# Optimization experiments

Measured on AMD Instinct MI355X. Metric: run time of the kernel, lower is better.

The kernel has to match this reference:

```python
import jax, jax.numpy as jnp
import numpy as np

N_NODES = 100000
N_EDGES = 1600000
D_FEAT = 32


def setup_inputs() -> dict:
    key = jax.random.key(0)
    kx, ke = jax.random.split(key)
    x = jax.random.normal(kx, (N_NODES, D_FEAT), dtype=jnp.float32)
    edge_index = jax.random.randint(ke, (2, N_EDGES), 0, N_NODES, dtype=jnp.int64)
    return {"x": x, "edge_index": edge_index}


def reference(x, edge_index):
    # flow='source_to_target': messages flow from edge_index[0] (j, source)
    # to edge_index[1] (i, target).
    src = edge_index[0]  # [E] source node per edge (j)
    dst = edge_index[1]  # [E] target node per edge (i)
    # __lift__: gather source-node features per edge -> message(x_j) = x_j
    msgs = jnp.take(x, src, axis=0)  # [E, D]
    # aggregate with aggr='add': scatter-sum messages onto target nodes
    out = jax.ops.segment_sum(msgs, dst, num_segments=x.shape[0])  # [N, D]
    # update: identity
    return out
```

## Files before the change

kernel.cpp:

```cpp
#include <hip/hip_runtime.h>


#define D_FEAT 32
#define BKT_SHIFT 7
#define BKT_NODES 128
#define CAPSH 4
#define CAP (1 << CAPSH)
#define ECAP 4096
#define OVFCAP 65536
typedef unsigned int u32;

__global__ void __launch_bounds__(512)
k_scatter4(const int* __restrict__ src, const int* __restrict__ dst,
           u32* __restrict__ cnt, u32* __restrict__ bin,
           u32* __restrict__ ovf, u32* __restrict__ ovf_cnt,
           int n_edges, int nb, int nsub, int chunk) {
    extern __shared__ u32 smem[];
    u32* s_stage = smem;
    u32* s_cur   = smem + ((size_t)nb << CAPSH);
    int blk = blockIdx.x, t = threadIdx.x;
    for (int i = t; i < nb; i += 512) s_cur[i] = 0u;
    __syncthreads();
    int beg = blk * chunk, end = min(beg + chunk, n_edges);
    for (int e = beg + t; e < end; e += 512) {
        u32 d = (u32)dst[e];
        u32 b = d >> BKT_SHIFT;
        u32 pos = atomicAdd(&s_cur[b], 1u);
        u32 packed = (u32)src[e] | ((d & (BKT_NODES - 1)) << 17);
        if (pos < (u32)CAP) {
            s_stage[(b << CAPSH) + pos] = packed;
        } else {
            u32 g = atomicAdd(ovf_cnt, 1u);
            if (g < OVFCAP) { ovf[2 * g] = packed; ovf[2 * g + 1] = b; }
        }
    }
    __syncthreads();
    {
        int nquads = (nb << CAPSH) >> 2;
        uint4* gq = (uint4*)(bin + (((size_t)blk * nb) << CAPSH));
        const uint4* sq = (const uint4*)s_stage;
        for (int i = t; i < nquads; i += 512) gq[i] = sq[i];
    }
    u32* row = cnt + (size_t)blk * nb;
    for (int i = t; i < nb; i += 512) row[i] = min(s_cur[i], (u32)CAP);
}

__global__ void __launch_bounds__(512)
k_gather4(const float* __restrict__ x, const u32* __restrict__ cnt,
          const u32* __restrict__ bin, const u32* __restrict__ ovf,
          const u32* __restrict__ ovf_cnt, float* __restrict__ out,
          int n_nodes, int nb, int nsub) {
    __shared__ u32 s_cnt[512];
    __shared__ u32 s_sb[512];
    __shared__ u32 s_base[513];
    __shared__ u32 s_ent[ECAP];
    __shared__ u32 s_srt[ECAP];
    __shared__ u32 s_off[BKT_NODES + 1];
    __shared__ u32 s_cur[BKT_NODES];
    __shared__ u32 s_scan[BKT_NODES];
    int b = blockIdx.x, t = threadIdx.x;
    int node0 = b * BKT_NODES;
    const float4* x4 = (const float4*)x;
    const uint4* bin4 = (const uint4*)bin;
    int q = t & 7;
    int n0 = t >> 3;
    float4 a0 = make_float4(0.f, 0.f, 0.f, 0.f);
    float4 a1 = make_float4(0.f, 0.f, 0.f, 0.f);

    u32 c = 0u;
    if (t < nsub) c = min(cnt[(size_t)t * nb + b], (u32)CAP);
    s_cnt[t] = c;
    s_sb[t] = c;
    __syncthreads();
    for (int off = 1; off < 512; off <<= 1) {
        u32 y = (t >= off) ? s_sb[t - off] : 0u;
        __syncthreads();
        if (t >= off) s_sb[t] += y;
        __syncthreads();
    }
    s_base[t] = s_sb[t] - c;
    if (t == 511) s_base[512] = s_sb[511];
    __syncthreads();

    int subA = 0;
    u32 baseA = 0u;
    while (subA < nsub) {
        int lo = subA + 1, hi = nsub;
        while (lo < hi) {
            int mid = (lo + hi + 1) >> 1;
            if (s_base[mid] - baseA <= (u32)ECAP) lo = mid; else hi = mid - 1;
        }
        int subB = lo;
        int m = (int)(s_base[subB] - baseA);

        {
            int quads = (subB - subA) << (CAPSH - 2);
            for (int i = t; i < quads; i += 512) {
                int sub = subA + (i >> (CAPSH - 2));
                int k4 = i & ((1 << (CAPSH - 2)) - 1);
                int slot0 = k4 << 2;
                u32 cn = s_cnt[sub];
                if ((u32)slot0 < cn) {
                    uint4 v = bin4[(((size_t)sub * nb + b) << (CAPSH - 2)) + k4];
                    u32 base = (s_base[sub] - baseA) + slot0;
                    s_ent[base] = v.x;
                    if ((u32)(slot0 + 1) < cn) s_ent[base + 1] = v.y;
                    if ((u32)(slot0 + 2) < cn) s_ent[base + 2] = v.z;
                    if ((u32)(slot0 + 3) < cn) s_ent[base + 3] = v.w;
                }
            }
        }
        if (t < BKT_NODES) s_cur[t] = 0u;
        __syncthreads();

        for (int i = t; i < m; i += 512) atomicAdd(&s_cur[s_ent[i] >> 17], 1u);
        __syncthreads();
        u32 v = 0u;
        if (t < BKT_NODES) { v = s_cur[t]; s_scan[t] = v; }
        __syncthreads();
        for (int off = 1; off < BKT_NODES; off <<= 1) {
            u32 y = 0u;
            if (t < BKT_NODES && t >= off) y = s_scan[t - off];
            __syncthreads();
            if (t < BKT_NODES && t >= off) s_scan[t] += y;
            __syncthreads();
        }
        if (t < BKT_NODES) { u32 ex = s_scan[t] - v; s_off[t] = ex; s_cur[t] = ex; }
        if (t == BKT_NODES - 1) s_off[BKT_NODES] = s_scan[BKT_NODES - 1];
        __syncthreads();
        for (int i = t; i < m; i += 512) {
            u32 p = s_ent[i];
            u32 pos = atomicAdd(&s_cur[p >> 17], 1u);
            s_srt[pos] = p & 0x1FFFFu;
        }
        __syncthreads();

        {
            u32 j = s_off[n0], j1 = s_off[n0 + 1];
            for (; j + 3 < j1; j += 4) {
                float4 xa = x4[(size_t)s_srt[j] * 8 + q];
                float4 xb = x4[(size_t)s_srt[j + 1] * 8 + q];
                float4 xc = x4[(size_t)s_srt[j + 2] * 8 + q];
                float4 xd = x4[(size_t)s_srt[j + 3] * 8 + q];
                a0.x += xa.x + xb.x + xc.x + xd.x;
                a0.y += xa.y + xb.y + xc.y + xd.y;
                a0.z += xa.z + xb.z + xc.z + xd.z;
                a0.w += xa.w + xb.w + xc.w + xd.w;
            }
            for (; j < j1; ++j) {
                float4 xa = x4[(size_t)s_srt[j] * 8 + q];
                a0.x += xa.x; a0.y += xa.y; a0.z += xa.z; a0.w += xa.w;
            }
            j = s_off[n0 + 64]; j1 = s_off[n0 + 65];
            for (; j + 3 < j1; j += 4) {
                float4 xa = x4[(size_t)s_srt[j] * 8 + q];
                float4 xb = x4[(size_t)s_srt[j + 1] * 8 + q];
                float4 xc = x4[(size_t)s_srt[j + 2] * 8 + q];
                float4 xd = x4[(size_t)s_srt[j + 3] * 8 + q];
                a1.x += xa.x + xb.x + xc.x + xd.x;
                a1.y += xa.y + xb.y + xc.y + xd.y;
                a1.z += xa.z + xb.z + xc.z + xd.z;
                a1.w += xa.w + xb.w + xc.w + xd.w;
            }
            for (; j < j1; ++j) {
                float4 xa = x4[(size_t)s_srt[j] * 8 + q];
                a1.x += xa.x; a1.y += xa.y; a1.z += xa.z; a1.w += xa.w;
            }
        }
        __syncthreads();
        subA = subB;
        baseA = s_base[subB];
    }

    u32 novf = min(*ovf_cnt, (u32)OVFCAP);
    for (u32 i = 0; i < novf; ++i) {
        if (ovf[2 * i + 1] == (u32)b) {
            u32 p = ovf[2 * i];
            u32 dl = p >> 17;
            if (dl == (u32)n0 || dl == (u32)(n0 + 64)) {
                float4 xv = x4[(size_t)(p & 0x1FFFFu) * 8 + q];
                if (dl == (u32)n0) { a0.x += xv.x; a0.y += xv.y; a0.z += xv.z; a0.w += xv.w; }
                else               { a1.x += xv.x; a1.y += xv.y; a1.z += xv.z; a1.w += xv.w; }
            }
        }
    }

    float4* o4 = (float4*)out;
    if (node0 + n0 < n_nodes)      o4[(size_t)node0 * 8 + t] = a0;
    if (node0 + n0 + 64 < n_nodes) o4[(size_t)node0 * 8 + 512 + t] = a1;
}


__global__ void __launch_bounds__(256)
mp_zero_kernel(float* __restrict__ out, int n) {
    int i = blockIdx.x * blockDim.x + threadIdx.x;
    if (i < n) out[i] = 0.0f;
}

__global__ void __launch_bounds__(256)
mp_scatter_kernel(const float* __restrict__ x, const int* __restrict__ src,
                  const int* __restrict__ dst, float* __restrict__ out,
                  int n_edges) {
    int idx = blockIdx.x * blockDim.x + threadIdx.x;
    if (idx >= n_edges * 8) return;
    int e = idx >> 3;
    int c = idx & 7;
    const float4 v = *reinterpret_cast<const float4*>(x + (size_t)src[e] * D_FEAT + c * 4);
    float* o = out + (size_t)dst[e] * D_FEAT + c * 4;
    unsafeAtomicAdd(o + 0, v.x);
    unsafeAtomicAdd(o + 1, v.y);
    unsafeAtomicAdd(o + 2, v.z);
    unsafeAtomicAdd(o + 3, v.w);
}


extern "C" void kernel_launch(void* const* d_in, const int* in_sizes, int n_in,
                              void* d_out, int out_size, void* d_ws, size_t ws_size,
                              hipStream_t stream) {
    const float* x = (const float*)d_in[0];
    const int* edge_index = (const int*)d_in[1];
    int n_edges = in_sizes[1] / 2;
    const int* src = edge_index;
    const int* dst = edge_index + n_edges;
    float* out = (float*)d_out;
    int n_nodes = out_size / D_FEAT;

    int nb = (n_nodes + BKT_NODES - 1) >> BKT_SHIFT;

    size_t sc_lds = ((size_t)nb * CAP + nb) * sizeof(u32);

    if (n_nodes <= (1 << 17) && sc_lds <= 64 * 1024) {
        const int ncand[3] = {512, 384, 256};
        for (int ci = 0; ci < 3; ++ci) {
            int nsub = ncand[ci];
            int chunk = (n_edges + nsub - 1) / nsub;
            size_t need = ((size_t)nsub * nb
                           + 16
                           + 2 * (size_t)OVFCAP
                           + (((size_t)nsub * nb) << CAPSH))
                          * sizeof(u32);
            if (need > ws_size) continue;

            u32* cnt     = (u32*)d_ws;
            u32* ovf_cnt = cnt + (size_t)nsub * nb;
            u32* ovf     = ovf_cnt + 16;
            u32* bin     = ovf + 2 * (size_t)OVFCAP;

            hipMemsetAsync(ovf_cnt, 0, sizeof(u32), stream);
            k_scatter4<<<nsub, 512, sc_lds, stream>>>(src, dst, cnt, bin, ovf, ovf_cnt,
                                                      n_edges, nb, nsub, chunk);
            k_gather4<<<nb, 512, 0, stream>>>(x, cnt, bin, ovf, ovf_cnt, out,
                                              n_nodes, nb, nsub);
            return;
        }
    }

    mp_zero_kernel<<<(out_size + 255) / 256, 256, 0, stream>>>(out, out_size);
    int total_thr = n_edges * 8;
    mp_scatter_kernel<<<(total_thr + 255) / 256, 256, 0, stream>>>(x, src, dst, out, n_edges);
}
```

Measured before the change: 116.3 us.

## Transpose bin layout, per-block overflow buffers, wave-shuffle scans, drop memset

The staging bins are now stored bucket-major (bucket, sub-block), so each gather block reads one contiguous region, and the scatter only writes quads that hold valid entries. The global overflow counter and its memset launch are replaced by per-block overflow buffers with LDS counters. The gather's overflow scan is skipped when no block overflowed. The LDS Hillis-Steele scans with many barriers become wavefront shuffle scans. The trade-off is a smaller overflow capacity per block (512), which is more likely to be exceeded for skewed inputs.

Measured after the change: 114.4 us, median of 2. About the same (-1.7%).

```diff
diff --git a/kernel.cpp b/kernel.cpp
--- a/kernel.cpp
+++ b/kernel.cpp
@@ -7,19 +7,21 @@
 #define CAPSH 4
 #define CAP (1 << CAPSH)
 #define ECAP 4096
-#define OVFCAP 65536
+#define OVFB 512
 typedef unsigned int u32;
 
 __global__ void __launch_bounds__(512)
-k_scatter4(const int* __restrict__ src, const int* __restrict__ dst,
+k_scatter5(const int* __restrict__ src, const int* __restrict__ dst,
            u32* __restrict__ cnt, u32* __restrict__ bin,
-           u32* __restrict__ ovf, u32* __restrict__ ovf_cnt,
+           u32* __restrict__ ovfb, u32* __restrict__ ovfn,
            int n_edges, int nb, int nsub, int chunk) {
     extern __shared__ u32 smem[];
     u32* s_stage = smem;
     u32* s_cur   = smem + ((size_t)nb << CAPSH);
+    __shared__ u32 s_ovf_n;
     int blk = blockIdx.x, t = threadIdx.x;
     for (int i = t; i < nb; i += 512) s_cur[i] = 0u;
+    if (t == 0) s_ovf_n = 0u;
     __syncthreads();
     int beg = blk * chunk, end = min(beg + chunk, n_edges);
     for (int e = beg + t; e < end; e += 512) {
@@ -30,35 +32,46 @@
         if (pos < (u32)CAP) {
             s_stage[(b << CAPSH) + pos] = packed;
         } else {
-            u32 g = atomicAdd(ovf_cnt, 1u);
-            if (g < OVFCAP) { ovf[2 * g] = packed; ovf[2 * g + 1] = b; }
+            u32 g = atomicAdd(&s_ovf_n, 1u);
+            if (g < (u32)OVFB) {
+                ovfb[((size_t)blk * OVFB + g) * 2]     = packed;
+                ovfb[((size_t)blk * OVFB + g) * 2 + 1] = (u32)b;
+            }
         }
     }
     __syncthreads();
     {
-        int nquads = (nb << CAPSH) >> 2;
-        uint4* gq = (uint4*)(bin + (((size_t)blk * nb) << CAPSH));
         const uint4* sq = (const uint4*)s_stage;
-        for (int i = t; i < nquads; i += 512) gq[i] = sq[i];
+        uint4* gq = (uint4*)bin;
+        int nquads = nb << (CAPSH - 2);
+        for (int i = t; i < nquads; i += 512) {
+            int b  = i >> (CAPSH - 2);
+            int k4 = i & ((1 << (CAPSH - 2)) - 1);
+            u32 cn = min(s_cur[b], (u32)CAP);
+            if ((u32)(k4 << 2) < cn)
+                gq[(((size_t)b * nsub + blk) << (CAPSH - 2)) + k4] = sq[i];
+        }
     }
     u32* row = cnt + (size_t)blk * nb;
     for (int i = t; i < nb; i += 512) row[i] = min(s_cur[i], (u32)CAP);
+    if (t == 0) ovfn[blk] = min(s_ovf_n, (u32)OVFB);
 }
 
 __global__ void __launch_bounds__(512)
-k_gather4(const float* __restrict__ x, const u32* __restrict__ cnt,
-          const u32* __restrict__ bin, const u32* __restrict__ ovf,
-          const u32* __restrict__ ovf_cnt, float* __restrict__ out,
+k_gather5(const float* __restrict__ x, const u32* __restrict__ cnt,
+          const u32* __restrict__ bin, const u32* __restrict__ ovfb,
+          const u32* __restrict__ ovfn, float* __restrict__ out,
           int n_nodes, int nb, int nsub) {
     __shared__ u32 s_cnt[512];
-    __shared__ u32 s_sb[512];
     __shared__ u32 s_base[513];
+    __shared__ u32 s_wsum[8];
     __shared__ u32 s_ent[ECAP];
     __shared__ u32 s_srt[ECAP];
     __shared__ u32 s_off[BKT_NODES + 1];
     __shared__ u32 s_cur[BKT_NODES];
-    __shared__ u32 s_scan[BKT_NODES];
+    __shared__ u32 s_has;
     int b = blockIdx.x, t = threadIdx.x;
+    int lane = t & 63, wid = t >> 6;
     int node0 = b * BKT_NODES;
     const float4* x4 = (const float4*)x;
     const uint4* bin4 = (const uint4*)bin;
@@ -67,19 +80,28 @@
     float4 a0 = make_float4(0.f, 0.f, 0.f, 0.f);
     float4 a1 = make_float4(0.f, 0.f, 0.f, 0.f);
 
-    u32 c = 0u;
-    if (t < nsub) c = min(cnt[(size_t)t * nb + b], (u32)CAP);
+    u32 c = (t < nsub) ? min(cnt[(size_t)t * nb + b], (u32)CAP) : 0u;
+    u32 myovf = (t < nsub) ? ovfn[t] : 0u;
     s_cnt[t] = c;
-    s_sb[t] = c;
-    __syncthreads();
-    for (int off = 1; off < 512; off <<= 1) {
-        u32 y = (t >= off) ? s_sb[t - off] : 0u;
-        __syncthreads();
-        if (t >= off) s_sb[t] += y;
-        __syncthreads();
-    }
-    s_base[t] = s_sb[t] - c;
-    if (t == 511) s_base[512] = s_sb[511];
+    if (t == 0) s_has = 0u;
+    u32 s = c;
+    #pragma unroll
+    for (int off = 1; off < 64; off <<= 1) {
+        u32 y = __shfl_up(s, off, 64);
+        if (lane >= off) s += y;
+    }
+    if (lane == 63) s_wsum[wid] = s;
+    __syncthreads();
+    if (t == 0) {
+        u32 run = 0u;
+        #pragma unroll
+        for (int w = 0; w < 8; ++w) { u32 v = s_wsum[w]; s_wsum[w] = run; run += v; }
+    }
+    if (myovf) atomicOr(&s_has, 1u);
+    __syncthreads();
+    u32 incl = s + s_wsum[wid];
+    s_base[t] = incl - c;
+    if (t == 511) s_base[512] = incl;
     __syncthreads();
 
     int subA = 0;
@@ -95,13 +117,13 @@
 
         {
             int quads = (subB - subA) << (CAPSH - 2);
+            size_t qbase = ((size_t)b * nsub + subA) << (CAPSH - 2);
             for (int i = t; i < quads; i += 512) {
                 int sub = subA + (i >> (CAPSH - 2));
-                int k4 = i & ((1 << (CAPSH - 2)) - 1);
-                int slot0 = k4 << 2;
+                int slot0 = (i & ((1 << (CAPSH - 2)) - 1)) << 2;
                 u32 cn = s_cnt[sub];
                 if ((u32)slot0 < cn) {
-                    uint4 v = bin4[(((size_t)sub * nb + b) << (CAPSH - 2)) + k4];
+                    uint4 v = bin4[qbase + i];
                     u32 base = (s_base[sub] - baseA) + slot0;
                     s_ent[base] = v.x;
                     if ((u32)(slot0 + 1) < cn) s_ent[base + 1] = v.y;
@@ -115,19 +137,22 @@
 
         for (int i = t; i < m; i += 512) atomicAdd(&s_cur[s_ent[i] >> 17], 1u);
         __syncthreads();
-        u32 v = 0u;
-        if (t < BKT_NODES) { v = s_cur[t]; s_scan[t] = v; }
-        __syncthreads();
-        for (int off = 1; off < BKT_NODES; off <<= 1) {
-            u32 y = 0u;
-            if (t < BKT_NODES && t >= off) y = s_scan[t - off];
-            __syncthreads();
-            if (t < BKT_NODES && t >= off) s_scan[t] += y;
-            __syncthreads();
-        }
-        if (t < BKT_NODES) { u32 ex = s_scan[t] - v; s_off[t] = ex; s_cur[t] = ex; }
-        if (t == BKT_NODES - 1) s_off[BKT_NODES] = s_scan[BKT_NODES - 1];
-        __syncthreads();
+
+        if (wid == 0) {
+            u32 v0 = s_cur[2 * lane], v1 = s_cur[2 * lane + 1];
+            u32 ps = v0 + v1;
+            #pragma unroll
+            for (int off = 1; off < 64; off <<= 1) {
+                u32 y = __shfl_up(ps, off, 64);
+                if (lane >= off) ps += y;
+            }
+            u32 ex = ps - (v0 + v1);
+            s_off[2 * lane] = ex;     s_cur[2 * lane] = ex;
+            s_off[2 * lane + 1] = ex + v0; s_cur[2 * lane + 1] = ex + v0;
+            if (lane == 63) s_off[BKT_NODES] = ps;
+        }
+        __syncthreads();
+
         for (int i = t; i < m; i += 512) {
             u32 p = s_ent[i];
             u32 pos = atomicAdd(&s_cur[p >> 17], 1u);
@@ -172,15 +197,20 @@
         baseA = s_base[subB];
     }
 
-    u32 novf = min(*ovf_cnt, (u32)OVFCAP);
-    for (u32 i = 0; i < novf; ++i) {
-        if (ovf[2 * i + 1] == (u32)b) {
-            u32 p = ovf[2 * i];
-            u32 dl = p >> 17;
-            if (dl == (u32)n0 || dl == (u32)(n0 + 64)) {
-                float4 xv = x4[(size_t)(p & 0x1FFFFu) * 8 + q];
-                if (dl == (u32)n0) { a0.x += xv.x; a0.y += xv.y; a0.z += xv.z; a0.w += xv.w; }
-                else               { a1.x += xv.x; a1.y += xv.y; a1.z += xv.z; a1.w += xv.w; }
+    if (s_has) {
+        for (int sub = 0; sub < nsub; ++sub) {
+            u32 n = ovfn[sub];
+            for (u32 i = 0; i < n; ++i) {
+                u32 ob = ovfb[((size_t)sub * OVFB + i) * 2 + 1];
+                if (ob == (u32)b) {
+                    u32 p = ovfb[((size_t)sub * OVFB + i) * 2];
+                    u32 dl = p >> 17;
+                    if (dl == (u32)n0 || dl == (u32)(n0 + 64)) {
+                        float4 xv = x4[(size_t)(p & 0x1FFFFu) * 8 + q];
+                        if (dl == (u32)n0) { a0.x += xv.x; a0.y += xv.y; a0.z += xv.z; a0.w += xv.w; }
+                        else               { a1.x += xv.x; a1.y += xv.y; a1.z += xv.z; a1.w += xv.w; }
+                    }
+                }
             }
         }
     }
@@ -235,21 +265,20 @@
             int nsub = ncand[ci];
             int chunk = (n_edges + nsub - 1) / nsub;
             size_t need = ((size_t)nsub * nb
-                           + 16
-                           + 2 * (size_t)OVFCAP
-                           + (((size_t)nsub * nb) << CAPSH))
+                           + 512
+                           + 2 * (size_t)nsub * OVFB
+                           + (((size_t)nb * nsub) << CAPSH))
                           * sizeof(u32);
             if (need > ws_size) continue;
 
-            u32* cnt     = (u32*)d_ws;
-            u32* ovf_cnt = cnt + (size_t)nsub * nb;
-            u32* ovf     = ovf_cnt + 16;
-            u32* bin     = ovf + 2 * (size_t)OVFCAP;
-
-            hipMemsetAsync(ovf_cnt, 0, sizeof(u32), stream);
-            k_scatter4<<<nsub, 512, sc_lds, stream>>>(src, dst, cnt, bin, ovf, ovf_cnt,
+            u32* cnt  = (u32*)d_ws;
+            u32* ovfn = cnt + (size_t)nsub * nb;
+            u32* ovfb = ovfn + 512;
+            u32* bin  = ovfb + 2 * (size_t)nsub * OVFB;
+
+            k_scatter5<<<nsub, 512, sc_lds, stream>>>(src, dst, cnt, bin, ovfb, ovfn,
                                                       n_edges, nb, nsub, chunk);
-            k_gather4<<<nb, 512, 0, stream>>>(x, cnt, bin, ovf, ovf_cnt, out,
+            k_gather5<<<nb, 512, 0, stream>>>(x, cnt, bin, ovfb, ovfn, out,
                                               n_nodes, nb, nsub);
             return;
         }
```
